# Optimization experiments

Measured on AMD Instinct MI355X. Metric: run time of the kernel, lower is better.

The kernel has to match this reference:

```python
import jax, jax.numpy as jnp
import numpy as np

H = 0.5
EPS = 1e-08


def setup_inputs() -> dict:
    key = jax.random.key(0)
    k1, k2, k3 = jax.random.split(key, 3)
    B, in_dim, n_rules, out_dim = 16384, 64, 128, 32
    X = jax.random.normal(k1, (B, in_dim), dtype=jnp.float32)
    centers = jax.random.normal(k2, (in_dim, n_rules), dtype=jnp.float32)
    sigmas = jnp.ones((in_dim, n_rules), dtype=jnp.float32)
    W = jax.random.normal(k3, (out_dim, (in_dim + 1) * n_rules), dtype=jnp.float32) * 0.02
    b = jnp.zeros((out_dim,), dtype=jnp.float32)
    return {"X": X, "centers": centers, "sigmas": sigmas, "W": W, "b": b}


def reference(X, centers, sigmas, W, b):
    # HTSK firing levels: mean-style scaled Gaussian log-memberships summed over in_dim
    scale = H / sigmas ** 2 + EPS                      # [in_dim, n_rules]
    diff = X[:, :, None] - centers[None, :, :]          # [B, in_dim, n_rules]
    logits = jnp.sum(-(diff ** 2) * scale, axis=1)      # [B, n_rules]
    frs = jax.nn.softmax(logits, axis=1)                # [B, n_rules]
    B = X.shape[0]
    # order=1 consequent input: rule-major outer product, then raw firing levels
    xr = (frs[:, :, None] * X[:, None, :]).reshape(B, -1)  # [B, n_rules*in_dim]
    Z = jnp.concatenate([xr, frs], axis=1)               # [B, n_rules*(in_dim+1)]
    output = Z @ W.T + b                                 # [B, out_dim]
    return output, frs
```

## Files before the change

kernel.cpp:

```cpp
#include <hip/hip_runtime.h>


#define H_CONST 0.5f
#define EPS_CONST 1e-8f
#define NROWS 16384
#define NRULES 128
#define WCOLS 8320

typedef _Float16 half8 __attribute__((ext_vector_type(8)));
typedef float floatx4 __attribute__((ext_vector_type(4)));

#define MFMA16(a, b, c) __builtin_amdgcn_mfma_f32_16x16x32_f16((a), (b), (c), 0, 0, 0)

#define WFRAG_OFF 0
#define W0FRAG_OFF 262144
#define BMAT_OFF   (262144 + 4096)
#define KVEC_BYTE_OFF 630784
#define WS_BYTES_NEEDED (630784 + 512)

__global__ __launch_bounds__(256) void prep_kernel(
    const float* __restrict__ centers, const float* __restrict__ sigmas,
    const float* __restrict__ W, _Float16* __restrict__ wsh, float* __restrict__ kvec)
{
    __shared__ float sBuf[32 * 68];
    const int t = threadIdx.x;
    const int b = blockIdx.x;

    if (b < 128) {
        const int r = b;
        {
            int o = t >> 3, seg = t & 7;
            const float* g = W + o * WCOLS + r * 64 + seg * 8;
            floatx4 a = *(const floatx4*)g;
            floatx4 c = *(const floatx4*)(g + 4);
            *(floatx4*)(sBuf + o * 68 + seg * 8) = a;
            *(floatx4*)(sBuf + o * 68 + seg * 8 + 4) = c;
        }
        __syncthreads();
        {
            int L = t & 63, nt = (t >> 6) & 1, s = t >> 7;
            int o = nt * 16 + (L & 15);
            int ib = s * 32 + ((L >> 4) & 3) * 8;
            floatx4 fa = *(const floatx4*)(sBuf + o * 68 + ib);
            floatx4 fb = *(const floatx4*)(sBuf + o * 68 + ib + 4);
            half8 h;
#pragma unroll
            for (int k = 0; k < 8; ++k) h[k] = (_Float16)((k < 4) ? fa[k & 3] : fb[k & 3]);
            *(half8*)(wsh + WFRAG_OFF + r * 2048 + t * 8) = h;
        }
    } else if (b < 136) {
        const int nt = b - 128;
        float* sS = sBuf;
        float* sC = sBuf + 1088;
        {
            int i = t >> 2, c0 = (t & 3) * 4;
            floatx4 sg4 = *(const floatx4*)(sigmas + i * NRULES + nt * 16 + c0);
            floatx4 ct4 = *(const floatx4*)(centers + i * NRULES + nt * 16 + c0);
#pragma unroll
            for (int k = 0; k < 4; ++k) { sS[i * 17 + c0 + k] = sg4[k]; sC[i * 17 + c0 + k] = ct4[k]; }
        }
        __syncthreads();
#pragma unroll
        for (int kk = 0; kk < 3; ++kk) {
            int unit = t + kk * 256;
            int s = unit >> 6, L = unit & 63;
            int q = (L >> 4) & 3, nl = L & 15;
            int g = s >> 1;
            int i0 = (s & 1) * 32 + q * 8;
            half8 h;
#pragma unroll
            for (int j = 0; j < 8; ++j) {
                int i = i0 + j;
                float sg = sS[i * 17 + nl];
                float S = H_CONST / (sg * sg) + EPS_CONST;
                float c = sC[i * 17 + nl];
                float CS2 = 2.0f * c * S;
                _Float16 v;
                if (g == 0 || g == 2) v = -(_Float16)S;
                else if (g == 1) { _Float16 sh = (_Float16)S; v = -(_Float16)(S - (float)sh); }
                else if (g == 3 || g == 5) v = (_Float16)CS2;
                else { _Float16 ch = (_Float16)CS2; v = (_Float16)(CS2 - (float)ch); }
                h[j] = v;
            }
            *(half8*)(wsh + BMAT_OFF + ((s * 8 + nt) * 64 + L) * 8) = h;
        }
    } else {
#pragma unroll
        for (int kk = 0; kk < 2; ++kk) {
            int unit = t + kk * 256;
            int s = unit >> 7, nt = (unit >> 6) & 1, L = unit & 63;
            int q = (L >> 4) & 3;
            int o = nt * 16 + (L & 15);
            half8 h;
#pragma unroll
            for (int j = 0; j < 8; ++j) {
                int r = s * 32 + q * 8 + j;
                h[j] = (_Float16)W[o * WCOLS + 8192 + r];
            }
            *(half8*)(wsh + W0FRAG_OFF + ((s * 2 + nt) * 64 + L) * 8) = h;
        }
        if (t < 128) {
            int r = t;
            float acc = 0.f;
#pragma unroll 8
            for (int i = 0; i < 64; ++i) {
                float sg = sigmas[i * NRULES + r];
                float S = H_CONST / (sg * sg) + EPS_CONST;
                float c = centers[i * NRULES + r];
                acc += c * c * S;
            }
            kvec[r] = acc;
        }
    }
}

__global__ __launch_bounds__(256) void k1_frs(
    const float* __restrict__ X, const float* __restrict__ bias,
    const _Float16* __restrict__ wsh, const float* __restrict__ kvec,
    float* __restrict__ out, float* __restrict__ frs_out)
{
    __shared__ _Float16 sXh[32 * 64];
    __shared__ _Float16 sXl[32 * 64];
    __shared__ _Float16 sX2h[32 * 64];
    __shared__ _Float16 sX2l[32 * 64];
    __shared__ float sU[32 * 132];

    const int t = threadIdx.x;
    const int w = t >> 6;
    const int L = t & 63;
    const int m = L & 15;
    const int q = L >> 4;
    const int row0 = blockIdx.x * 32;

    {
        int row = t >> 3, uc = t & 7;
        const float* gx = X + (row0 + row) * 64 + uc * 8;
        floatx4 xa = *(const floatx4*)gx;
        floatx4 xb = *(const floatx4*)(gx + 4);
        int base = row * 64 + (uc ^ (row & 7)) * 8;
        half8 vh, vl, v2h, v2l;
#pragma unroll
        for (int k = 0; k < 8; ++k) {
            float x = (k < 4) ? xa[k & 3] : xb[k & 3];
            _Float16 xh = (_Float16)x;
            _Float16 xl2 = (_Float16)(x - (float)xh);
            float x2 = x * x;
            _Float16 x2h = (_Float16)x2;
            _Float16 x2l = (_Float16)(x2 - (float)x2h);
            vh[k] = xh; vl[k] = xl2; v2h[k] = x2h; v2l[k] = x2l;
        }
        *(half8*)(sXh + base) = vh;
        *(half8*)(sXl + base) = vl;
        *(half8*)(sX2h + base) = v2h;
        *(half8*)(sX2l + base) = v2l;
    }
    __syncthreads();

    floatx4 lacc[2][2];
#pragma unroll
    for (int mt = 0; mt < 2; ++mt)
#pragma unroll
        for (int n = 0; n < 2; ++n) lacc[mt][n] = (floatx4){0.f, 0.f, 0.f, 0.f};

    const _Float16* Bm = wsh + BMAT_OFF;
#pragma unroll
    for (int s = 0; s < 12; ++s) {
        const _Float16* arr = (s < 4) ? sX2h : (s < 6) ? sX2l : (s < 10) ? sXh : sXl;
        int phys = (((s & 1) << 2) | q) ^ (m & 7);
        half8 b0 = *(const half8*)(Bm + ((s * 8 + 2 * w + 0) * 64 + L) * 8);
        half8 b1 = *(const half8*)(Bm + ((s * 8 + 2 * w + 1) * 64 + L) * 8);
#pragma unroll
        for (int mt = 0; mt < 2; ++mt) {
            half8 a = *(const half8*)(arr + (mt * 16 + m) * 64 + phys * 8);
            lacc[mt][0] = MFMA16(a, b0, lacc[mt][0]);
            lacc[mt][1] = MFMA16(a, b1, lacc[mt][1]);
        }
    }
    float kv0 = kvec[(2 * w + 0) * 16 + m];
    float kv1 = kvec[(2 * w + 1) * 16 + m];

#pragma unroll
    for (int mt = 0; mt < 2; ++mt)
#pragma unroll
        for (int ntl = 0; ntl < 2; ++ntl)
#pragma unroll
            for (int reg = 0; reg < 4; ++reg) {
                int rl = mt * 16 + q * 4 + reg;
                int col = (2 * w + ntl) * 16 + m;
                sU[rl * 132 + col] = lacc[mt][ntl][reg] - (ntl ? kv1 : kv0);
            }
    __syncthreads();

    {
        int row = t >> 3, l8 = t & 7;
        int base = row * 132 + l8 * 16;
        float v[16];
        float mx = -1e30f;
#pragma unroll
        for (int k = 0; k < 16; ++k) { v[k] = sU[base + k]; mx = fmaxf(mx, v[k]); }
        mx = fmaxf(mx, __shfl_xor(mx, 1));
        mx = fmaxf(mx, __shfl_xor(mx, 2));
        mx = fmaxf(mx, __shfl_xor(mx, 4));
        float sum = 0.f;
#pragma unroll
        for (int k = 0; k < 16; ++k) { v[k] = __expf(v[k] - mx); sum += v[k]; }
        sum += __shfl_xor(sum, 1);
        sum += __shfl_xor(sum, 2);
        sum += __shfl_xor(sum, 4);
        float inv = 1.0f / sum;
        float* gf = frs_out + (row0 + row) * 128 + l8 * 16;
#pragma unroll
        for (int c = 0; c < 4; ++c) {
            floatx4 o4;
#pragma unroll
            for (int k = 0; k < 4; ++k) o4[k] = v[c * 4 + k] * inv;
            *(floatx4*)(gf + c * 4) = o4;
        }
    }

    {
        int ro = t >> 3, c0 = (t & 7) * 4;
        floatx4 b4 = *(const floatx4*)(bias + c0);
        *(floatx4*)(out + (row0 + ro) * 32 + c0) = b4;
    }
}

__global__ __launch_bounds__(256) void k2_gemm(
    const float* __restrict__ X, const float* __restrict__ frs32,
    const _Float16* __restrict__ wsh, float* __restrict__ out)
{
    __shared__ _Float16 sXf[128 * 64];
    __shared__ _Float16 sF[128 * 40];

    const int t = threadIdx.x;
    const int w = t >> 6;
    const int L = t & 63;
    const int m = L & 15;
    const int q = L >> 4;
    const int rb = blockIdx.x >> 2;
    const int g = blockIdx.x & 3;
    const int row0 = rb * 128;

    {
        int row = t >> 1, hf = t & 1;
        const float* gx = X + (row0 + row) * 64 + hf * 32;
#pragma unroll
        for (int c = 0; c < 4; ++c) {
            int uc = hf * 4 + c;
            floatx4 a = *(const floatx4*)(gx + c * 8);
            floatx4 bb = *(const floatx4*)(gx + c * 8 + 4);
            half8 h;
#pragma unroll
            for (int k = 0; k < 8; ++k) h[k] = (_Float16)((k < 4) ? a[k & 3] : bb[k & 3]);
            *(half8*)(sXf + row * 64 + (uc ^ (row & 7)) * 8) = h;
        }
        const float* gfr = frs32 + (row0 + row) * 128 + g * 32 + hf * 16;
#pragma unroll
        for (int c = 0; c < 2; ++c) {
            floatx4 a = *(const floatx4*)(gfr + c * 8);
            floatx4 bb = *(const floatx4*)(gfr + c * 8 + 4);
            half8 h;
#pragma unroll
            for (int k = 0; k < 8; ++k) h[k] = (_Float16)((k < 4) ? a[k & 3] : bb[k & 3]);
            *(half8*)(sF + row * 40 + hf * 16 + c * 8) = h;
        }
    }
    __syncthreads();

    half8 xf[2][2];
#pragma unroll
    for (int mtl = 0; mtl < 2; ++mtl) {
        int mt = 2 * w + mtl;
#pragma unroll
        for (int s = 0; s < 2; ++s) {
            int phys = ((s << 2) | q) ^ (m & 7);
            xf[mtl][s] = *(const half8*)(sXf + (mt * 16 + m) * 64 + phys * 8);
        }
    }

    floatx4 oacc[2][2];
#pragma unroll
    for (int mtl = 0; mtl < 2; ++mtl)
#pragma unroll
        for (int n = 0; n < 2; ++n) oacc[mtl][n] = (floatx4){0.f, 0.f, 0.f, 0.f};

    const _Float16* Wf = wsh + WFRAG_OFF;
    const _Float16* W0f = wsh + W0FRAG_OFF;

#pragma unroll 4
    for (int rr = 0; rr < 32; ++rr) {
        int r = g * 32 + rr;
        const _Float16* bp = Wf + r * 2048;
        half8 b00 = *(const half8*)(bp + (0 * 64 + L) * 8);
        half8 b01 = *(const half8*)(bp + (1 * 64 + L) * 8);
        half8 b10 = *(const half8*)(bp + (2 * 64 + L) * 8);
        half8 b11 = *(const half8*)(bp + (3 * 64 + L) * 8);
#pragma unroll
        for (int mtl = 0; mtl < 2; ++mtl) {
            int rowi = (2 * w + mtl) * 16 + m;
            _Float16 f = sF[rowi * 40 + rr];
            half8 fs;
#pragma unroll
            for (int k = 0; k < 8; ++k) fs[k] = f;
            half8 a0 = fs * xf[mtl][0];
            half8 a1 = fs * xf[mtl][1];
            oacc[mtl][0] = MFMA16(a0, b00, oacc[mtl][0]);
            oacc[mtl][0] = MFMA16(a1, b10, oacc[mtl][0]);
            oacc[mtl][1] = MFMA16(a0, b01, oacc[mtl][1]);
            oacc[mtl][1] = MFMA16(a1, b11, oacc[mtl][1]);
        }
    }

    {
        half8 b0 = *(const half8*)(W0f + ((g * 2 + 0) * 64 + L) * 8);
        half8 b1 = *(const half8*)(W0f + ((g * 2 + 1) * 64 + L) * 8);
#pragma unroll
        for (int mtl = 0; mtl < 2; ++mtl) {
            int rowi = (2 * w + mtl) * 16 + m;
            half8 a = *(const half8*)(sF + rowi * 40 + q * 8);
            oacc[mtl][0] = MFMA16(a, b0, oacc[mtl][0]);
            oacc[mtl][1] = MFMA16(a, b1, oacc[mtl][1]);
        }
    }

#pragma unroll
    for (int mtl = 0; mtl < 2; ++mtl)
#pragma unroll
        for (int ntl = 0; ntl < 2; ++ntl)
#pragma unroll
            for (int reg = 0; reg < 4; ++reg) {
                int rowo = (2 * w + mtl) * 16 + q * 4 + reg;
                int colo = ntl * 16 + m;
                atomicAdd(out + (row0 + rowo) * 32 + colo, oacc[mtl][ntl][reg]);
            }
}

extern "C" void kernel_launch(void* const* d_in, const int* in_sizes, int n_in,
                              void* d_out, int out_size, void* d_ws, size_t ws_size,
                              hipStream_t stream) {
    const float* X = (const float*)d_in[0];
    const float* centers = (const float*)d_in[1];
    const float* sigmas = (const float*)d_in[2];
    const float* W = (const float*)d_in[3];
    const float* b = (const float*)d_in[4];
    float* outp = (float*)d_out;
    float* frs_out = outp + NROWS * 32;
    if (ws_size < (size_t)WS_BYTES_NEEDED) return;
    _Float16* wsh = (_Float16*)d_ws;
    float* kvec = (float*)((char*)d_ws + KVEC_BYTE_OFF);

    prep_kernel<<<137, 256, 0, stream>>>(centers, sigmas, W, wsh, kvec);
    k1_frs<<<NROWS / 32, 256, 0, stream>>>(X, b, wsh, kvec, outp, frs_out);
    k2_gemm<<<(NROWS / 128) * 4, 256, 0, stream>>>(X, frs_out, wsh, outp);
}
```

Baseline: 97.64 us.

## Fuse firing-level softmax and consequent GEMM into one kernel, drop atomics

Merges the softmax/firing-level kernel and the consequent GEMM kernel into a single kernel that keeps fp16 firing levels in shared memory and reuses the already-staged fp16 X tile. Each block of 32 rows splits the 128 rules across two wave pairs and reduces their partial outputs through shared memory, writing the output with bias directly instead of using atomics. This removes a kernel launch, the global re-read of frs and X, and the atomic adds. In exchange, each block runs the full 128-rule reduction, so every wave streams all of its W fragments per 32 rows, giving less reuse of W per block than the previous 128-row tiles.

```diff
diff --git a/kernel.cpp b/kernel.cpp
--- a/kernel.cpp
+++ b/kernel.cpp
@@ -114,7 +114,7 @@
     }
 }
 
-__global__ __launch_bounds__(256) void k1_frs(
+__global__ __launch_bounds__(256) void main_fused(
     const float* __restrict__ X, const float* __restrict__ bias,
     const _Float16* __restrict__ wsh, const float* __restrict__ kvec,
     float* __restrict__ out, float* __restrict__ frs_out)
@@ -124,6 +124,7 @@
     __shared__ _Float16 sX2h[32 * 64];
     __shared__ _Float16 sX2l[32 * 64];
     __shared__ float sU[32 * 132];
+    __shared__ _Float16 sF[32 * 136];
 
     const int t = threadIdx.x;
     const int w = t >> 6;
@@ -209,130 +210,95 @@
         sum += __shfl_xor(sum, 4);
         float inv = 1.0f / sum;
         float* gf = frs_out + (row0 + row) * 128 + l8 * 16;
+        half8 h0, h1;
 #pragma unroll
         for (int c = 0; c < 4; ++c) {
             floatx4 o4;
 #pragma unroll
-            for (int k = 0; k < 4; ++k) o4[k] = v[c * 4 + k] * inv;
+            for (int k = 0; k < 4; ++k) {
+                float f = v[c * 4 + k] * inv;
+                o4[k] = f;
+                if (c < 2) h0[c * 4 + k] = (_Float16)f; else h1[(c - 2) * 4 + k] = (_Float16)f;
+            }
             *(floatx4*)(gf + c * 4) = o4;
         }
-    }
-
-    {
-        int ro = t >> 3, c0 = (t & 7) * 4;
-        floatx4 b4 = *(const floatx4*)(bias + c0);
-        *(floatx4*)(out + (row0 + ro) * 32 + c0) = b4;
-    }
-}
-
-__global__ __launch_bounds__(256) void k2_gemm(
-    const float* __restrict__ X, const float* __restrict__ frs32,
-    const _Float16* __restrict__ wsh, float* __restrict__ out)
-{
-    __shared__ _Float16 sXf[128 * 64];
-    __shared__ _Float16 sF[128 * 40];
-
-    const int t = threadIdx.x;
-    const int w = t >> 6;
-    const int L = t & 63;
-    const int m = L & 15;
-    const int q = L >> 4;
-    const int rb = blockIdx.x >> 2;
-    const int g = blockIdx.x & 3;
-    const int row0 = rb * 128;
-
-    {
-        int row = t >> 1, hf = t & 1;
-        const float* gx = X + (row0 + row) * 64 + hf * 32;
-#pragma unroll
-        for (int c = 0; c < 4; ++c) {
-            int uc = hf * 4 + c;
-            floatx4 a = *(const floatx4*)(gx + c * 8);
-            floatx4 bb = *(const floatx4*)(gx + c * 8 + 4);
-            half8 h;
-#pragma unroll
-            for (int k = 0; k < 8; ++k) h[k] = (_Float16)((k < 4) ? a[k & 3] : bb[k & 3]);
-            *(half8*)(sXf + row * 64 + (uc ^ (row & 7)) * 8) = h;
-        }
-        const float* gfr = frs32 + (row0 + row) * 128 + g * 32 + hf * 16;
-#pragma unroll
-        for (int c = 0; c < 2; ++c) {
-            floatx4 a = *(const floatx4*)(gfr + c * 8);
-            floatx4 bb = *(const floatx4*)(gfr + c * 8 + 4);
-            half8 h;
-#pragma unroll
-            for (int k = 0; k < 8; ++k) h[k] = (_Float16)((k < 4) ? a[k & 3] : bb[k & 3]);
-            *(half8*)(sF + row * 40 + hf * 16 + c * 8) = h;
-        }
+        *(half8*)(sF + row * 136 + l8 * 16) = h0;
+        *(half8*)(sF + row * 136 + l8 * 16 + 8) = h1;
     }
     __syncthreads();
 
-    half8 xf[2][2];
-#pragma unroll
-    for (int mtl = 0; mtl < 2; ++mtl) {
-        int mt = 2 * w + mtl;
-#pragma unroll
-        for (int s = 0; s < 2; ++s) {
-            int phys = ((s << 2) | q) ^ (m & 7);
-            xf[mtl][s] = *(const half8*)(sXf + (mt * 16 + m) * 64 + phys * 8);
-        }
-    }
-
-    floatx4 oacc[2][2];
-#pragma unroll
-    for (int mtl = 0; mtl < 2; ++mtl)
-#pragma unroll
-        for (int n = 0; n < 2; ++n) oacc[mtl][n] = (floatx4){0.f, 0.f, 0.f, 0.f};
+    const int mt = w & 1;
+    const int rh = w >> 1;
+
+    half8 xf[2];
+#pragma unroll
+    for (int s = 0; s < 2; ++s) {
+        int phys = ((s << 2) | q) ^ (m & 7);
+        xf[s] = *(const half8*)(sXh + (mt * 16 + m) * 64 + phys * 8);
+    }
+
+    floatx4 oacc[2];
+    oacc[0] = (floatx4){0.f, 0.f, 0.f, 0.f};
+    oacc[1] = (floatx4){0.f, 0.f, 0.f, 0.f};
 
     const _Float16* Wf = wsh + WFRAG_OFF;
     const _Float16* W0f = wsh + W0FRAG_OFF;
+    const int rowi = mt * 16 + m;
 
 #pragma unroll 4
-    for (int rr = 0; rr < 32; ++rr) {
-        int r = g * 32 + rr;
+    for (int rr = 0; rr < 64; ++rr) {
+        int r = rh * 64 + rr;
         const _Float16* bp = Wf + r * 2048;
         half8 b00 = *(const half8*)(bp + (0 * 64 + L) * 8);
         half8 b01 = *(const half8*)(bp + (1 * 64 + L) * 8);
         half8 b10 = *(const half8*)(bp + (2 * 64 + L) * 8);
         half8 b11 = *(const half8*)(bp + (3 * 64 + L) * 8);
-#pragma unroll
-        for (int mtl = 0; mtl < 2; ++mtl) {
-            int rowi = (2 * w + mtl) * 16 + m;
-            _Float16 f = sF[rowi * 40 + rr];
-            half8 fs;
-#pragma unroll
-            for (int k = 0; k < 8; ++k) fs[k] = f;
-            half8 a0 = fs * xf[mtl][0];
-            half8 a1 = fs * xf[mtl][1];
-            oacc[mtl][0] = MFMA16(a0, b00, oacc[mtl][0]);
-            oacc[mtl][0] = MFMA16(a1, b10, oacc[mtl][0]);
-            oacc[mtl][1] = MFMA16(a0, b01, oacc[mtl][1]);
-            oacc[mtl][1] = MFMA16(a1, b11, oacc[mtl][1]);
-        }
-    }
-
-    {
-        half8 b0 = *(const half8*)(W0f + ((g * 2 + 0) * 64 + L) * 8);
-        half8 b1 = *(const half8*)(W0f + ((g * 2 + 1) * 64 + L) * 8);
-#pragma unroll
-        for (int mtl = 0; mtl < 2; ++mtl) {
-            int rowi = (2 * w + mtl) * 16 + m;
-            half8 a = *(const half8*)(sF + rowi * 40 + q * 8);
-            oacc[mtl][0] = MFMA16(a, b0, oacc[mtl][0]);
-            oacc[mtl][1] = MFMA16(a, b1, oacc[mtl][1]);
-        }
-    }
-
-#pragma unroll
-    for (int mtl = 0; mtl < 2; ++mtl)
+        _Float16 f = sF[rowi * 136 + r];
+        half8 fs;
+#pragma unroll
+        for (int k = 0; k < 8; ++k) fs[k] = f;
+        half8 a0 = fs * xf[0];
+        half8 a1 = fs * xf[1];
+        oacc[0] = MFMA16(a0, b00, oacc[0]);
+        oacc[0] = MFMA16(a1, b10, oacc[0]);
+        oacc[1] = MFMA16(a0, b01, oacc[1]);
+        oacc[1] = MFMA16(a1, b11, oacc[1]);
+    }
+
+#pragma unroll
+    for (int sg = 0; sg < 2; ++sg) {
+        int s = 2 * rh + sg;
+        half8 a = *(const half8*)(sF + rowi * 136 + s * 32 + q * 8);
+        half8 b0 = *(const half8*)(W0f + ((s * 2 + 0) * 64 + L) * 8);
+        half8 b1 = *(const half8*)(W0f + ((s * 2 + 1) * 64 + L) * 8);
+        oacc[0] = MFMA16(a, b0, oacc[0]);
+        oacc[1] = MFMA16(a, b1, oacc[1]);
+    }
+
+    float* sR = sU;
+    if (rh == 1) {
 #pragma unroll
         for (int ntl = 0; ntl < 2; ++ntl)
 #pragma unroll
+            for (int reg = 0; reg < 4; ++reg)
+                sR[(mt * 16 + q * 4 + reg) * 33 + ntl * 16 + m] = oacc[ntl][reg];
+    }
+    __syncthreads();
+    if (rh == 0) {
+        float b0 = bias[m];
+        float b1 = bias[16 + m];
+#pragma unroll
+        for (int ntl = 0; ntl < 2; ++ntl) {
+            float bb = ntl ? b1 : b0;
+#pragma unroll
             for (int reg = 0; reg < 4; ++reg) {
-                int rowo = (2 * w + mtl) * 16 + q * 4 + reg;
-                int colo = ntl * 16 + m;
-                atomicAdd(out + (row0 + rowo) * 32 + colo, oacc[mtl][ntl][reg]);
-            }
+                int rloc = mt * 16 + q * 4 + reg;
+                int col = ntl * 16 + m;
+                float vv = oacc[ntl][reg] + sR[rloc * 33 + col] + bb;
+                out[(row0 + rloc) * 32 + col] = vv;
+            }
+        }
+    }
 }
 
 extern "C" void kernel_launch(void* const* d_in, const int* in_sizes, int n_in,
@@ -350,6 +316,5 @@
     float* kvec = (float*)((char*)d_ws + KVEC_BYTE_OFF);
 
     prep_kernel<<<137, 256, 0, stream>>>(centers, sigmas, W, wsh, kvec);
-    k1_frs<<<NROWS / 32, 256, 0, stream>>>(X, b, wsh, kvec, outp, frs_out);
-    k2_gemm<<<(NROWS / 128) * 4, 256, 0, stream>>>(X, frs_out, wsh, outp);
+    main_fused<<<NROWS / 32, 256, 0, stream>>>(X, b, wsh, kvec, outp, frs_out);
 }
```

Result: faster. 92.85 us (-4.9%).

## Halve per-block work in frs and GEMM kernels, prefetch W fragments

Applied to the files above, without the earlier changes.

k1_frs now handles 16 rows per block instead of 32, doubling its grid, and k2_gemm splits the rules into 8 groups of 16 instead of 4 groups of 32, doubling its grid and the number of atomic adds into the output. The GEMM loop is fully unrolled with one-step software prefetch of the W fragments, and the firing levels are loaded once into registers instead of per-iteration LDS reads. The bias-fragment MFMA is masked per lane group to fit the narrower rule slice. The aim is more blocks for occupancy and hidden load latency, at the cost of extra atomics and repeated X staging per block.

```diff
diff --git a/kernel.cpp b/kernel.cpp
--- a/kernel.cpp
+++ b/kernel.cpp
@@ -8,6 +8,7 @@
 #define WCOLS 8320
 
 typedef _Float16 half8 __attribute__((ext_vector_type(8)));
+typedef _Float16 half4 __attribute__((ext_vector_type(4)));
 typedef float floatx4 __attribute__((ext_vector_type(4)));
 
 #define MFMA16(a, b, c) __builtin_amdgcn_mfma_f32_16x16x32_f16((a), (b), (c), 0, 0, 0)
@@ -119,29 +120,29 @@
     const _Float16* __restrict__ wsh, const float* __restrict__ kvec,
     float* __restrict__ out, float* __restrict__ frs_out)
 {
-    __shared__ _Float16 sXh[32 * 64];
-    __shared__ _Float16 sXl[32 * 64];
-    __shared__ _Float16 sX2h[32 * 64];
-    __shared__ _Float16 sX2l[32 * 64];
-    __shared__ float sU[32 * 132];
+    __shared__ _Float16 sXh[16 * 64];
+    __shared__ _Float16 sXl[16 * 64];
+    __shared__ _Float16 sX2h[16 * 64];
+    __shared__ _Float16 sX2l[16 * 64];
+    __shared__ float sU[16 * 132];
 
     const int t = threadIdx.x;
     const int w = t >> 6;
     const int L = t & 63;
     const int m = L & 15;
     const int q = L >> 4;
-    const int row0 = blockIdx.x * 32;
+    const int row0 = blockIdx.x * 16;
 
     {
-        int row = t >> 3, uc = t & 7;
-        const float* gx = X + (row0 + row) * 64 + uc * 8;
+        int u = t >> 1, hs = t & 1;
+        int row = u >> 3, uc = u & 7;
+        const float* gx = X + (row0 + row) * 64 + uc * 8 + hs * 4;
         floatx4 xa = *(const floatx4*)gx;
-        floatx4 xb = *(const floatx4*)(gx + 4);
-        int base = row * 64 + (uc ^ (row & 7)) * 8;
-        half8 vh, vl, v2h, v2l;
-#pragma unroll
-        for (int k = 0; k < 8; ++k) {
-            float x = (k < 4) ? xa[k & 3] : xb[k & 3];
+        int base = row * 64 + (uc ^ (row & 7)) * 8 + hs * 4;
+        half4 vh, vl, v2h, v2l;
+#pragma unroll
+        for (int k = 0; k < 4; ++k) {
+            float x = xa[k];
             _Float16 xh = (_Float16)x;
             _Float16 xl2 = (_Float16)(x - (float)xh);
             float x2 = x * x;
@@ -149,18 +150,15 @@
             _Float16 x2l = (_Float16)(x2 - (float)x2h);
             vh[k] = xh; vl[k] = xl2; v2h[k] = x2h; v2l[k] = x2l;
         }
-        *(half8*)(sXh + base) = vh;
-        *(half8*)(sXl + base) = vl;
-        *(half8*)(sX2h + base) = v2h;
-        *(half8*)(sX2l + base) = v2l;
+        *(half4*)(sXh + base) = vh;
+        *(half4*)(sXl + base) = vl;
+        *(half4*)(sX2h + base) = v2h;
+        *(half4*)(sX2l + base) = v2l;
     }
     __syncthreads();
 
-    floatx4 lacc[2][2];
-#pragma unroll
-    for (int mt = 0; mt < 2; ++mt)
-#pragma unroll
-        for (int n = 0; n < 2; ++n) lacc[mt][n] = (floatx4){0.f, 0.f, 0.f, 0.f};
+    floatx4 lacc0 = (floatx4){0.f, 0.f, 0.f, 0.f};
+    floatx4 lacc1 = (floatx4){0.f, 0.f, 0.f, 0.f};
 
     const _Float16* Bm = wsh + BMAT_OFF;
 #pragma unroll
@@ -169,59 +167,52 @@
         int phys = (((s & 1) << 2) | q) ^ (m & 7);
         half8 b0 = *(const half8*)(Bm + ((s * 8 + 2 * w + 0) * 64 + L) * 8);
         half8 b1 = *(const half8*)(Bm + ((s * 8 + 2 * w + 1) * 64 + L) * 8);
-#pragma unroll
-        for (int mt = 0; mt < 2; ++mt) {
-            half8 a = *(const half8*)(arr + (mt * 16 + m) * 64 + phys * 8);
-            lacc[mt][0] = MFMA16(a, b0, lacc[mt][0]);
-            lacc[mt][1] = MFMA16(a, b1, lacc[mt][1]);
-        }
+        half8 a = *(const half8*)(arr + m * 64 + phys * 8);
+        lacc0 = MFMA16(a, b0, lacc0);
+        lacc1 = MFMA16(a, b1, lacc1);
     }
     float kv0 = kvec[(2 * w + 0) * 16 + m];
     float kv1 = kvec[(2 * w + 1) * 16 + m];
 
 #pragma unroll
-    for (int mt = 0; mt < 2; ++mt)
-#pragma unroll
-        for (int ntl = 0; ntl < 2; ++ntl)
-#pragma unroll
-            for (int reg = 0; reg < 4; ++reg) {
-                int rl = mt * 16 + q * 4 + reg;
-                int col = (2 * w + ntl) * 16 + m;
-                sU[rl * 132 + col] = lacc[mt][ntl][reg] - (ntl ? kv1 : kv0);
-            }
+    for (int reg = 0; reg < 4; ++reg) {
+        int rl = q * 4 + reg;
+        sU[rl * 132 + (2 * w + 0) * 16 + m] = lacc0[reg] - kv0;
+        sU[rl * 132 + (2 * w + 1) * 16 + m] = lacc1[reg] - kv1;
+    }
     __syncthreads();
 
     {
-        int row = t >> 3, l8 = t & 7;
-        int base = row * 132 + l8 * 16;
-        float v[16];
+        int row = t >> 4, l16 = t & 15;
+        int base = row * 132 + l16 * 8;
+        float v[8];
         float mx = -1e30f;
 #pragma unroll
-        for (int k = 0; k < 16; ++k) { v[k] = sU[base + k]; mx = fmaxf(mx, v[k]); }
+        for (int k = 0; k < 8; ++k) { v[k] = sU[base + k]; mx = fmaxf(mx, v[k]); }
         mx = fmaxf(mx, __shfl_xor(mx, 1));
         mx = fmaxf(mx, __shfl_xor(mx, 2));
         mx = fmaxf(mx, __shfl_xor(mx, 4));
+        mx = fmaxf(mx, __shfl_xor(mx, 8));
         float sum = 0.f;
 #pragma unroll
-        for (int k = 0; k < 16; ++k) { v[k] = __expf(v[k] - mx); sum += v[k]; }
+        for (int k = 0; k < 8; ++k) { v[k] = __expf(v[k] - mx); sum += v[k]; }
         sum += __shfl_xor(sum, 1);
         sum += __shfl_xor(sum, 2);
         sum += __shfl_xor(sum, 4);
+        sum += __shfl_xor(sum, 8);
         float inv = 1.0f / sum;
-        float* gf = frs_out + (row0 + row) * 128 + l8 * 16;
-#pragma unroll
-        for (int c = 0; c < 4; ++c) {
-            floatx4 o4;
-#pragma unroll
-            for (int k = 0; k < 4; ++k) o4[k] = v[c * 4 + k] * inv;
-            *(floatx4*)(gf + c * 4) = o4;
-        }
-    }
-
-    {
-        int ro = t >> 3, c0 = (t & 7) * 4;
+        float* gf = frs_out + (row0 + row) * 128 + l16 * 8;
+        floatx4 f0, f1;
+#pragma unroll
+        for (int k = 0; k < 4; ++k) { f0[k] = v[k] * inv; f1[k] = v[k + 4] * inv; }
+        *(floatx4*)gf = f0;
+        *(floatx4*)(gf + 4) = f1;
+    }
+
+    if (t < 128) {
+        int row = t >> 3, c0 = (t & 7) * 4;
         floatx4 b4 = *(const floatx4*)(bias + c0);
-        *(floatx4*)(out + (row0 + ro) * 32 + c0) = b4;
+        *(floatx4*)(out + (row0 + row) * 32 + c0) = b4;
     }
 }
 
@@ -230,15 +221,15 @@
     const _Float16* __restrict__ wsh, float* __restrict__ out)
 {
     __shared__ _Float16 sXf[128 * 64];
-    __shared__ _Float16 sF[128 * 40];
+    __shared__ _Float16 sF[128 * 18];
 
     const int t = threadIdx.x;
     const int w = t >> 6;
     const int L = t & 63;
     const int m = L & 15;
     const int q = L >> 4;
-    const int rb = blockIdx.x >> 2;
-    const int g = blockIdx.x & 3;
+    const int rb = blockIdx.x >> 3;
+    const int g = blockIdx.x & 7;
     const int row0 = rb * 128;
 
     {
@@ -254,18 +245,18 @@
             for (int k = 0; k < 8; ++k) h[k] = (_Float16)((k < 4) ? a[k & 3] : bb[k & 3]);
             *(half8*)(sXf + row * 64 + (uc ^ (row & 7)) * 8) = h;
         }
-        const float* gfr = frs32 + (row0 + row) * 128 + g * 32 + hf * 16;
-#pragma unroll
-        for (int c = 0; c < 2; ++c) {
-            floatx4 a = *(const floatx4*)(gfr + c * 8);
-            floatx4 bb = *(const floatx4*)(gfr + c * 8 + 4);
-            half8 h;
-#pragma unroll
-            for (int k = 0; k < 8; ++k) h[k] = (_Float16)((k < 4) ? a[k & 3] : bb[k & 3]);
-            *(half8*)(sF + row * 40 + hf * 16 + c * 8) = h;
-        }
+        const float* gfr = frs32 + (row0 + row) * 128 + g * 16 + hf * 8;
+        floatx4 a = *(const floatx4*)gfr;
+        floatx4 bb = *(const floatx4*)(gfr + 4);
+        half8 h;
+#pragma unroll
+        for (int k = 0; k < 8; ++k) h[k] = (_Float16)((k < 4) ? a[k & 3] : bb[k & 3]);
+        *(half8*)(sF + row * 18 + hf * 8) = h;
     }
     __syncthreads();
+
+    const int r0w0 = (2 * w + 0) * 16 + m;
+    const int r0w1 = (2 * w + 1) * 16 + m;
 
     half8 xf[2][2];
 #pragma unroll
@@ -278,6 +269,11 @@
         }
     }
 
+    half8 fvA0 = *(const half8*)(sF + r0w0 * 18);
+    half8 fvB0 = *(const half8*)(sF + r0w0 * 18 + 8);
+    half8 fvA1 = *(const half8*)(sF + r0w1 * 18);
+    half8 fvB1 = *(const half8*)(sF + r0w1 * 18 + 8);
+
     floatx4 oacc[2][2];
 #pragma unroll
     for (int mtl = 0; mtl < 2; ++mtl)
@@ -287,40 +283,51 @@
     const _Float16* Wf = wsh + WFRAG_OFF;
     const _Float16* W0f = wsh + W0FRAG_OFF;
 
-#pragma unroll 4
-    for (int rr = 0; rr < 32; ++rr) {
-        int r = g * 32 + rr;
-        const _Float16* bp = Wf + r * 2048;
-        half8 b00 = *(const half8*)(bp + (0 * 64 + L) * 8);
-        half8 b01 = *(const half8*)(bp + (1 * 64 + L) * 8);
-        half8 b10 = *(const half8*)(bp + (2 * 64 + L) * 8);
-        half8 b11 = *(const half8*)(bp + (3 * 64 + L) * 8);
-#pragma unroll
-        for (int mtl = 0; mtl < 2; ++mtl) {
-            int rowi = (2 * w + mtl) * 16 + m;
-            _Float16 f = sF[rowi * 40 + rr];
-            half8 fs;
-#pragma unroll
-            for (int k = 0; k < 8; ++k) fs[k] = f;
-            half8 a0 = fs * xf[mtl][0];
-            half8 a1 = fs * xf[mtl][1];
-            oacc[mtl][0] = MFMA16(a0, b00, oacc[mtl][0]);
-            oacc[mtl][0] = MFMA16(a1, b10, oacc[mtl][0]);
-            oacc[mtl][1] = MFMA16(a0, b01, oacc[mtl][1]);
-            oacc[mtl][1] = MFMA16(a1, b11, oacc[mtl][1]);
-        }
+#define LDW(r, slot) (*(const half8*)(Wf + (r) * 2048 + ((slot) * 64 + L) * 8))
+
+    half8 b00 = LDW(g * 16, 0), b01 = LDW(g * 16, 1);
+    half8 b10 = LDW(g * 16, 2), b11 = LDW(g * 16, 3);
+
+#pragma unroll
+    for (int rr = 0; rr < 16; ++rr) {
+        half8 c00 = b00, c01 = b01, c10 = b10, c11 = b11;
+        if (rr < 15) {
+            int rn = g * 16 + rr + 1;
+            b00 = LDW(rn, 0); b01 = LDW(rn, 1); b10 = LDW(rn, 2); b11 = LDW(rn, 3);
+        }
+        _Float16 f0 = (rr < 8) ? fvA0[rr & 7] : fvB0[rr & 7];
+        _Float16 f1 = (rr < 8) ? fvA1[rr & 7] : fvB1[rr & 7];
+        half8 fs0, fs1;
+#pragma unroll
+        for (int k = 0; k < 8; ++k) { fs0[k] = f0; fs1[k] = f1; }
+        half8 a00 = fs0 * xf[0][0];
+        half8 a01 = fs0 * xf[0][1];
+        half8 a10 = fs1 * xf[1][0];
+        half8 a11 = fs1 * xf[1][1];
+        oacc[0][0] = MFMA16(a00, c00, oacc[0][0]);
+        oacc[0][0] = MFMA16(a01, c10, oacc[0][0]);
+        oacc[0][1] = MFMA16(a00, c01, oacc[0][1]);
+        oacc[0][1] = MFMA16(a01, c11, oacc[0][1]);
+        oacc[1][0] = MFMA16(a10, c00, oacc[1][0]);
+        oacc[1][0] = MFMA16(a11, c10, oacc[1][0]);
+        oacc[1][1] = MFMA16(a10, c01, oacc[1][1]);
+        oacc[1][1] = MFMA16(a11, c11, oacc[1][1]);
     }
 
     {
-        half8 b0 = *(const half8*)(W0f + ((g * 2 + 0) * 64 + L) * 8);
-        half8 b1 = *(const half8*)(W0f + ((g * 2 + 1) * 64 + L) * 8);
-#pragma unroll
-        for (int mtl = 0; mtl < 2; ++mtl) {
-            int rowi = (2 * w + mtl) * 16 + m;
-            half8 a = *(const half8*)(sF + rowi * 40 + q * 8);
-            oacc[mtl][0] = MFMA16(a, b0, oacc[mtl][0]);
-            oacc[mtl][1] = MFMA16(a, b1, oacc[mtl][1]);
-        }
+        int s = g >> 1;
+        bool valid = ((q >> 1) == (g & 1));
+        half8 zero;
+#pragma unroll
+        for (int k = 0; k < 8; ++k) zero[k] = (_Float16)0.f;
+        half8 wb0 = *(const half8*)(W0f + ((s * 2 + 0) * 64 + L) * 8);
+        half8 wb1 = *(const half8*)(W0f + ((s * 2 + 1) * 64 + L) * 8);
+        half8 a0 = valid ? *(const half8*)(sF + r0w0 * 18 + (q & 1) * 8) : zero;
+        half8 a1 = valid ? *(const half8*)(sF + r0w1 * 18 + (q & 1) * 8) : zero;
+        oacc[0][0] = MFMA16(a0, wb0, oacc[0][0]);
+        oacc[0][1] = MFMA16(a0, wb1, oacc[0][1]);
+        oacc[1][0] = MFMA16(a1, wb0, oacc[1][0]);
+        oacc[1][1] = MFMA16(a1, wb1, oacc[1][1]);
     }
 
 #pragma unroll
@@ -333,6 +340,7 @@
                 int colo = ntl * 16 + m;
                 atomicAdd(out + (row0 + rowo) * 32 + colo, oacc[mtl][ntl][reg]);
             }
+#undef LDW
 }
 
 extern "C" void kernel_launch(void* const* d_in, const int* in_sizes, int n_in,
@@ -350,6 +358,6 @@
     float* kvec = (float*)((char*)d_ws + KVEC_BYTE_OFF);
 
     prep_kernel<<<137, 256, 0, stream>>>(centers, sigmas, W, wsh, kvec);
-    k1_frs<<<NROWS / 32, 256, 0, stream>>>(X, b, wsh, kvec, outp, frs_out);
-    k2_gemm<<<(NROWS / 128) * 4, 256, 0, stream>>>(X, frs_out, wsh, outp);
+    k1_frs<<<NROWS / 16, 256, 0, stream>>>(X, b, wsh, kvec, outp, frs_out);
+    k2_gemm<<<(NROWS / 128) * 8, 256, 0, stream>>>(X, frs_out, wsh, outp);
 }
```

Measured after the change: 101.7 us. 4.2% more time.
